# Kernel optimization log

Hardware: AMD Instinct MI355X
Metric: run time of the kernel (lower is better)

## Reference

```python
import jax, jax.numpy as jnp
import numpy as np

N_USER = 100000
N_ITEM = 50000
EMB = 64
LAYERS = 3
N_INTER = 2000000
BATCH = 4096


def setup_inputs() -> dict:
    key = jax.random.key(0)
    ks = jax.random.split(key, 12)
    N = N_USER + N_ITEM
    # bipartite interactions u -> i, symmetrized
    u = jax.random.randint(ks[0], (N_INTER,), 0, N_USER, dtype=jnp.int32)
    i = jax.random.randint(ks[1], (N_INTER,), 0, N_ITEM, dtype=jnp.int32) + N_USER
    edge_src = jnp.concatenate([u, i])
    edge_dst = jnp.concatenate([i, u])
    # symmetric normalization D^-1/2 A D^-1/2 (as in getSparseGraph)
    deg = jnp.bincount(edge_dst, length=N).astype(jnp.float32)
    d_inv_sqrt = jnp.where(deg > 0, jax.lax.rsqrt(jnp.maximum(deg, 1.0)), 0.0)
    edge_w = d_inv_sqrt[edge_src] * d_inv_sqrt[edge_dst]
    s = 1.0 / np.sqrt(EMB)  # xavier-ish scale
    inp = {
        "user_emb": jax.random.normal(ks[2], (N_USER, EMB), jnp.float32) * s,
        "item_emb": jax.random.normal(ks[3], (N_ITEM, EMB), jnp.float32) * s,
        "W_gc": jax.random.normal(ks[4], (LAYERS, EMB, EMB), jnp.float32) * s,
        "b_gc": jax.random.normal(ks[5], (LAYERS, 1, EMB), jnp.float32) * s,
        "W_bi": jax.random.normal(ks[6], (LAYERS, EMB, EMB), jnp.float32) * s,
        "b_bi": jax.random.normal(ks[7], (LAYERS, 1, EMB), jnp.float32) * s,
        "edge_w": edge_w,
        "edge_src": edge_src,
        "edge_dst": edge_dst,
        "users": jax.random.randint(ks[8], (BATCH,), 0, N_USER, dtype=jnp.int64),
        "pos_items": jax.random.randint(ks[9], (BATCH,), 0, N_ITEM, dtype=jnp.int64),
        "neg_items": jax.random.randint(ks[10], (BATCH,), 0, N_ITEM, dtype=jnp.int64),
    }
    return inp


def reference(user_emb, item_emb, W_gc, b_gc, W_bi, b_bi, edge_w,
              edge_src, edge_dst, users, pos_items, neg_items):
    n_user = user_emb.shape[0]
    N = n_user + item_emb.shape[0]
    ego = jnp.concatenate([user_emb, item_emb], axis=0)  # [N, d]
    all_embeddings = [ego]
    for k in range(W_gc.shape[0]):
        # SpMM: side = A_hat @ ego  (gather + weighted scatter-add)
        side = jax.ops.segment_sum(ego[edge_src] * edge_w[:, None], edge_dst,
                                   num_segments=N)
        sum_e = side @ W_gc[k] + b_gc[k]
        bi_e = (ego * side) @ W_bi[k] + b_bi[k]
        ego = jax.nn.leaky_relu(sum_e + bi_e, negative_slope=0.2)
        # dropout omitted (eval mode / identity for deterministic baseline)
        nrm = jnp.linalg.norm(ego, axis=1, keepdims=True)
        all_embeddings.append(ego / jnp.maximum(nrm, 1e-12))
    all_e = jnp.concatenate(all_embeddings, axis=1)  # [N, (L+1)*d]
    u_g = all_e[:n_user][users]
    i_g = all_e[n_user:]
    return (u_g, i_g[pos_items], i_g[neg_items])
```

## Files before the change

kernel.cpp:

```cpp
#include <hip/hip_runtime.h>

#define EMB 64
#define B2SHIFT 8
#define B2ROWS 256
#define MAXB 1024

typedef short v8s __attribute__((ext_vector_type(8)));
typedef float v4f __attribute__((ext_vector_type(4)));

__device__ __forceinline__ float b2f(unsigned short u) {
    return __uint_as_float(((unsigned int)u) << 16);
}
__device__ __forceinline__ float b2f_lo(unsigned int u) {
    return __uint_as_float(u << 16);
}
__device__ __forceinline__ float b2f_hi(unsigned int u) {
    return __uint_as_float(u & 0xFFFF0000u);
}
__device__ __forceinline__ unsigned short f2b(float f) {
    unsigned int u = __float_as_uint(f);
    u += 0x7FFF + ((u >> 16) & 1);
    return (unsigned short)(u >> 16);
}

__global__ void k_init_ego(const float* __restrict__ user_emb,
                           const float* __restrict__ item_emb,
                           const float* __restrict__ dsq,
                           unsigned short* __restrict__ egob,
                           unsigned short* __restrict__ egow,
                           unsigned short* __restrict__ all_eb,
                           int n_user, int N) {
    int idx = blockIdx.x * blockDim.x + threadIdx.x;
    int total = N * 16;
    if (idx >= total) return;
    int n = idx >> 4;
    int q = idx & 15;
    float4 v = (n < n_user)
        ? ((const float4*)user_emb)[idx]
        : ((const float4*)item_emb)[(size_t)(n - n_user) * 16 + q];
    float dn = dsq[n];
    unsigned int pb0 = (unsigned)f2b(v.x) | ((unsigned)f2b(v.y) << 16);
    unsigned int pb1 = (unsigned)f2b(v.z) | ((unsigned)f2b(v.w) << 16);
    unsigned int pw0 = (unsigned)f2b(dn * v.x) | ((unsigned)f2b(dn * v.y) << 16);
    unsigned int pw1 = (unsigned)f2b(dn * v.z) | ((unsigned)f2b(dn * v.w) << 16);
    unsigned int* egobd = (unsigned int*)egob;
    unsigned int* egowd = (unsigned int*)egow;
    egobd[idx * 2 + 0] = pb0;
    egobd[idx * 2 + 1] = pb1;
    egowd[idx * 2 + 0] = pw0;
    egowd[idx * 2 + 1] = pw1;
    unsigned int* ae = (unsigned int*)all_eb;
    __builtin_nontemporal_store(pb0, &ae[(size_t)n * 128 + q * 2 + 0]);
    __builtin_nontemporal_store(pb1, &ae[(size_t)n * 128 + q * 2 + 1]);
}

__global__ __launch_bounds__(256) void k_bhist(const int* __restrict__ dst,
                                               int* __restrict__ bins,
                                               int M, int nb2) {
    __shared__ int h[MAXB];
    for (int i = threadIdx.x; i < nb2; i += 256) h[i] = 0;
    __syncthreads();
    for (int e = blockIdx.x * 256 + threadIdx.x; e < M; e += gridDim.x * 256)
        atomicAdd(&h[dst[e] >> B2SHIFT], 1);
    __syncthreads();
    for (int i = threadIdx.x; i < nb2; i += 256)
        if (h[i]) atomicAdd(&bins[i], h[i]);
}

__global__ __launch_bounds__(1024) void k_bscan(const int* __restrict__ bins,
                                                int* __restrict__ boff,
                                                int* __restrict__ bcur,
                                                int* __restrict__ row_ptr,
                                                int P, int N) {
    __shared__ int buf[1024];
    int tid = threadIdx.x;
    int v = (tid < P) ? bins[tid] : 0;
    buf[tid] = v;
    __syncthreads();
    for (int d = 1; d < 1024; d <<= 1) {
        int add = (tid >= d) ? buf[tid - d] : 0;
        __syncthreads();
        buf[tid] += add;
        __syncthreads();
    }
    if (tid < P) {
        int excl = buf[tid] - v;
        boff[tid] = excl;
        bcur[tid] = excl;
    }
    if (tid == P - 1) {
        boff[P] = buf[tid];
        row_ptr[N] = buf[tid];
    }
}

__global__ __launch_bounds__(256) void k_bin(const int* __restrict__ src,
                                             const int* __restrict__ dst,
                                             int* __restrict__ bcur,
                                             int* __restrict__ binned,
                                             int M, int nb2) {
    __shared__ int hist[MAXB];
    __shared__ int runcur[MAXB];
    int chunk = (M + gridDim.x - 1) / gridDim.x;
    int lo = blockIdx.x * chunk;
    int hi = min(lo + chunk, M);
    for (int i = threadIdx.x; i < nb2; i += 256) hist[i] = 0;
    __syncthreads();
    for (int e = lo + threadIdx.x; e < hi; e += 256)
        atomicAdd(&hist[dst[e] >> B2SHIFT], 1);
    __syncthreads();
    for (int i = threadIdx.x; i < nb2; i += 256) {
        int c = hist[i];
        runcur[i] = c ? atomicAdd(&bcur[i], c) : 0;
    }
    __syncthreads();
    for (int e = lo + threadIdx.x; e < hi; e += 256) {
        int d = dst[e];
        int pos = atomicAdd(&runcur[d >> B2SHIFT], 1);
        binned[pos] = (src[e] << B2SHIFT) | (d & (B2ROWS - 1));
    }
}

__global__ __launch_bounds__(256) void k_csrb(const int* __restrict__ boff,
                                              const int* __restrict__ binned,
                                              int* __restrict__ row_ptr,
                                              float* __restrict__ dsq,
                                              int* __restrict__ csr, int N) {
    __shared__ int hist[B2ROWS];
    __shared__ int scan[B2ROWS];
    int b = blockIdx.x;
    int beg = boff[b], end = boff[b + 1];
    int tid = threadIdx.x;
    hist[tid] = 0;
    __syncthreads();
    for (int e = beg + tid; e < end; e += 256)
        atomicAdd(&hist[binned[e] & (B2ROWS - 1)], 1);
    __syncthreads();
    int c = hist[tid];
    scan[tid] = c;
    __syncthreads();
    for (int d = 1; d < B2ROWS; d <<= 1) {
        int add = (tid >= d) ? scan[tid - d] : 0;
        __syncthreads();
        scan[tid] += add;
        __syncthreads();
    }
    int excl = beg + scan[tid] - c;
    int node = (b << B2SHIFT) + tid;
    if (node < N) {
        row_ptr[node] = excl;
        dsq[node] = (c > 0) ? rsqrtf((float)c) : 0.0f;
    }
    __syncthreads();
    hist[tid] = excl;
    __syncthreads();
    for (int e = beg + tid; e < end; e += 256) {
        int v = binned[e];
        int pos = atomicAdd(&hist[v & (B2ROWS - 1)], 1);
        csr[pos] = v >> B2SHIFT;
    }
}

__global__ __launch_bounds__(256) void k_side(const int* __restrict__ row_ptr,
                                              const int* __restrict__ csr,
                                              const float* __restrict__ dsq,
                                              const unsigned short* __restrict__ egow,
                                              const unsigned short* __restrict__ egob,
                                              unsigned short* __restrict__ X, int N) {
    int wave = threadIdx.x >> 6;
    int lane = threadIdx.x & 63;
    int n = blockIdx.x * 4 + wave;
    if (n >= N) return;
    int beg = __builtin_amdgcn_readfirstlane(row_ptr[n]);
    int end = __builtin_amdgcn_readfirstlane(row_ptr[n + 1]);
    float a0 = 0.f, a1 = 0.f, a2 = 0.f, a3 = 0.f;
    int e = beg;
    for (; e + 16 <= end; e += 16) {
        int s0  = csr[e + 0],  s1  = csr[e + 1],  s2  = csr[e + 2],  s3  = csr[e + 3];
        int s4  = csr[e + 4],  s5  = csr[e + 5],  s6  = csr[e + 6],  s7  = csr[e + 7];
        int s8  = csr[e + 8],  s9  = csr[e + 9],  s10 = csr[e + 10], s11 = csr[e + 11];
        int s12 = csr[e + 12], s13 = csr[e + 13], s14 = csr[e + 14], s15 = csr[e + 15];
        float v0  = b2f(egow[(size_t)s0  * EMB + lane]);
        float v1  = b2f(egow[(size_t)s1  * EMB + lane]);
        float v2  = b2f(egow[(size_t)s2  * EMB + lane]);
        float v3  = b2f(egow[(size_t)s3  * EMB + lane]);
        float v4  = b2f(egow[(size_t)s4  * EMB + lane]);
        float v5  = b2f(egow[(size_t)s5  * EMB + lane]);
        float v6  = b2f(egow[(size_t)s6  * EMB + lane]);
        float v7  = b2f(egow[(size_t)s7  * EMB + lane]);
        float v8  = b2f(egow[(size_t)s8  * EMB + lane]);
        float v9  = b2f(egow[(size_t)s9  * EMB + lane]);
        float v10 = b2f(egow[(size_t)s10 * EMB + lane]);
        float v11 = b2f(egow[(size_t)s11 * EMB + lane]);
        float v12 = b2f(egow[(size_t)s12 * EMB + lane]);
        float v13 = b2f(egow[(size_t)s13 * EMB + lane]);
        float v14 = b2f(egow[(size_t)s14 * EMB + lane]);
        float v15 = b2f(egow[(size_t)s15 * EMB + lane]);
        a0 += v0;  a1 += v1;  a2 += v2;  a3 += v3;
        a0 += v4;  a1 += v5;  a2 += v6;  a3 += v7;
        a0 += v8;  a1 += v9;  a2 += v10; a3 += v11;
        a0 += v12; a1 += v13; a2 += v14; a3 += v15;
    }
    for (; e + 4 <= end; e += 4) {
        int s0 = csr[e + 0], s1 = csr[e + 1], s2 = csr[e + 2], s3 = csr[e + 3];
        float v0 = b2f(egow[(size_t)s0 * EMB + lane]);
        float v1 = b2f(egow[(size_t)s1 * EMB + lane]);
        float v2 = b2f(egow[(size_t)s2 * EMB + lane]);
        float v3 = b2f(egow[(size_t)s3 * EMB + lane]);
        a0 += v0; a1 += v1; a2 += v2; a3 += v3;
    }
    for (; e < end; ++e) {
        int s0 = csr[e];
        a0 += b2f(egow[(size_t)s0 * EMB + lane]);
    }
    float s = dsq[n] * ((a0 + a1) + (a2 + a3));
    float eg = b2f(egob[(size_t)n * EMB + lane]);
    X[(size_t)n * 128 + lane] = f2b(s);
    X[(size_t)n * 128 + 64 + lane] = f2b(s * eg);
}

__global__ __launch_bounds__(256, 2) void k_mt(
        const unsigned short* __restrict__ X,
        unsigned short* __restrict__ egob, unsigned short* __restrict__ egow,
        const float* __restrict__ dsq,
        const float* __restrict__ Wgc, const float* __restrict__ bgc,
        const float* __restrict__ Wbi, const float* __restrict__ bbi,
        unsigned short* __restrict__ all_eb, int N, int layer_col,
        int write_next) {
    __shared__ unsigned short sWT[64 * 136];
    __shared__ __align__(16) float sB[64];
    int tid = threadIdx.x;
    for (int i = tid; i < 64 * 64; i += 256) {
        int k = i >> 6, n = i & 63;
        sWT[n * 136 + k]      = f2b(Wgc[i]);
        sWT[n * 136 + 64 + k] = f2b(Wbi[i]);
    }
    if (tid < 64) sB[tid] = bgc[tid] + bbi[tid];
    __syncthreads();

    int wave = tid >> 6, lane = tid & 63;
    int q = lane >> 4, col = lane & 15;

    v8s Bf[4][4];
#pragma unroll
    for (int nt = 0; nt < 4; nt++)
#pragma unroll
        for (int kt = 0; kt < 4; kt++)
            Bf[nt][kt] = *(const v8s*)&sWT[(nt * 16 + col) * 136 + kt * 32 + q * 8];
    float4 bias[4];
#pragma unroll
    for (int nt = 0; nt < 4; nt++)
        bias[nt] = ((const float4*)sB)[nt * 4 + q];

    int nrt = (N + 15) >> 4;
    int rt0 = (blockIdx.x * 4 + wave) * 4;
    int rt1 = min(rt0 + 4, nrt);
    for (int t = rt0; t < rt1; t++) {
        int r0 = t << 4;
        int rowA = min(r0 + col, N - 1);
        v8s Af[4];
#pragma unroll
        for (int kt = 0; kt < 4; kt++)
            Af[kt] = *(const v8s*)&X[(size_t)rowA * 128 + kt * 32 + q * 8];
        v4f acc[4];
#pragma unroll
        for (int nt = 0; nt < 4; nt++)
            acc[nt] = (v4f){bias[nt].x, bias[nt].y, bias[nt].z, bias[nt].w};
#pragma unroll
        for (int kt = 0; kt < 4; kt++)
#pragma unroll
            for (int nt = 0; nt < 4; nt++)
                acc[nt] = __builtin_amdgcn_mfma_f32_16x16x32_bf16(
                    Bf[nt][kt], Af[kt], acc[nt], 0, 0, 0);
        int row = r0 + col;
        float vv[4][4];
        float ssq = 0.f;
#pragma unroll
        for (int nt = 0; nt < 4; nt++)
#pragma unroll
            for (int rg = 0; rg < 4; rg++) {
                float x = acc[nt][rg];
                x = x > 0.f ? x : 0.2f * x;
                vv[nt][rg] = x;
                ssq += x * x;
            }
        ssq += __shfl_xor(ssq, 16, 64);
        ssq += __shfl_xor(ssq, 32, 64);
        float inv = 1.0f / fmaxf(sqrtf(ssq), 1e-12f);
        if (row < N) {
            unsigned int* ae = (unsigned int*)all_eb;
            size_t aeBase = (size_t)row * 128 + (layer_col >> 1);
#pragma unroll
            for (int nt = 0; nt < 4; nt++) {
                int cd = (nt * 16 + q * 4) >> 1;
                unsigned int p0 = (unsigned)f2b(vv[nt][0] * inv) |
                                  ((unsigned)f2b(vv[nt][1] * inv) << 16);
                unsigned int p1 = (unsigned)f2b(vv[nt][2] * inv) |
                                  ((unsigned)f2b(vv[nt][3] * inv) << 16);
                __builtin_nontemporal_store(p0, &ae[aeBase + cd + 0]);
                __builtin_nontemporal_store(p1, &ae[aeBase + cd + 1]);
            }
            if (write_next) {
                float dn = dsq[row];
                unsigned int* eb = (unsigned int*)egob;
                unsigned int* ew = (unsigned int*)egow;
                size_t base = (size_t)row * 32;
#pragma unroll
                for (int nt = 0; nt < 4; nt++) {
                    int cd = (nt * 16 + q * 4) >> 1;
                    unsigned int b0 = (unsigned)f2b(vv[nt][0]) |
                                      ((unsigned)f2b(vv[nt][1]) << 16);
                    unsigned int b1 = (unsigned)f2b(vv[nt][2]) |
                                      ((unsigned)f2b(vv[nt][3]) << 16);
                    eb[base + cd + 0] = b0;
                    eb[base + cd + 1] = b1;
                    unsigned int w0 = (unsigned)f2b(vv[nt][0] * dn) |
                                      ((unsigned)f2b(vv[nt][1] * dn) << 16);
                    unsigned int w1 = (unsigned)f2b(vv[nt][2] * dn) |
                                      ((unsigned)f2b(vv[nt][3] * dn) << 16);
                    ew[base + cd + 0] = w0;
                    ew[base + cd + 1] = w1;
                }
            }
        }
    }
}

__global__ void k_gather(const unsigned short* __restrict__ all_eb,
                         const int* __restrict__ users,
                         const int* __restrict__ pos,
                         const int* __restrict__ neg,
                         float* __restrict__ out, int n_user, int batch) {
    int idx = blockIdx.x * blockDim.x + threadIdx.x;
    int total = batch * 64;
    if (idx >= 3 * total) return;
    int which = idx / total;
    int r = idx - which * total;
    int b = r >> 6;
    int q = r & 63;
    int node;
    if (which == 0) node = users[b];
    else if (which == 1) node = n_user + pos[b];
    else node = n_user + neg[b];
    const unsigned int* ae = (const unsigned int*)all_eb;
    unsigned int d0 = ae[(size_t)node * 128 + q * 2 + 0];
    unsigned int d1 = ae[(size_t)node * 128 + q * 2 + 1];
    float4 o;
    o.x = b2f_lo(d0);
    o.y = b2f_hi(d0);
    o.z = b2f_lo(d1);
    o.w = b2f_hi(d1);
    ((float4*)out)[idx] = o;
}

static inline size_t align256(size_t x) { return (x + 255) & ~(size_t)255; }

extern "C" void kernel_launch(void* const* d_in, const int* in_sizes, int n_in,
                              void* d_out, int out_size, void* d_ws, size_t ws_size,
                              hipStream_t stream) {
    const float* user_emb = (const float*)d_in[0];
    const float* item_emb = (const float*)d_in[1];
    const float* W_gc = (const float*)d_in[2];
    const float* b_gc = (const float*)d_in[3];
    const float* W_bi = (const float*)d_in[4];
    const float* b_bi = (const float*)d_in[5];
    const int* edge_src = (const int*)d_in[7];
    const int* edge_dst = (const int*)d_in[8];
    const int* users = (const int*)d_in[9];
    const int* pos = (const int*)d_in[10];
    const int* neg = (const int*)d_in[11];

    int n_user = in_sizes[0] / EMB;
    int n_item = in_sizes[1] / EMB;
    int N = n_user + n_item;
    int M = in_sizes[6];
    int layers = in_sizes[2] / (EMB * EMB);
    int batch = in_sizes[9];
    float* out = (float*)d_out;

    int nb2 = (N + B2ROWS - 1) >> B2SHIFT;
    int nrt = (N + 15) >> 4;

    char* p = (char*)d_ws;
    unsigned short* egob = (unsigned short*)p;   p += align256((size_t)N * EMB * 2);
    unsigned short* egow = (unsigned short*)p;   p += align256((size_t)N * EMB * 2);
    unsigned short* X = (unsigned short*)p;      p += align256((size_t)N * 128 * 2);
    unsigned short* all_eb = (unsigned short*)p; p += align256((size_t)N * 256 * 2);
    float* dsq = (float*)p;            p += align256((size_t)N * 4);
    int* row_ptr = (int*)p;            p += align256((size_t)(N + 1) * 4);
    int* bins = (int*)p;               p += align256((size_t)nb2 * 4);
    int* boff = (int*)p;               p += align256((size_t)(nb2 + 1) * 4);
    int* bcur = (int*)p;               p += align256((size_t)nb2 * 4);
    int* binned = (int*)p;             p += align256((size_t)M * 4);
    int* csr = (int*)p;                p += align256((size_t)M * 4);

    hipMemsetAsync(bins, 0, (size_t)nb2 * 4, stream);

    k_bhist<<<512, 256, 0, stream>>>(edge_dst, bins, M, nb2);
    k_bscan<<<1, 1024, 0, stream>>>(bins, boff, bcur, row_ptr, nb2, N);
    k_bin<<<512, 256, 0, stream>>>(edge_src, edge_dst, bcur, binned, M, nb2);
    k_csrb<<<nb2, 256, 0, stream>>>(boff, binned, row_ptr, dsq, csr, N);

    k_init_ego<<<(N * 16 + 255) / 256, 256, 0, stream>>>(
        user_emb, item_emb, dsq, egob, egow, all_eb, n_user, N);

    for (int k = 0; k < layers; k++) {
        k_side<<<(N + 3) / 4, 256, 0, stream>>>(row_ptr, csr, dsq, egow, egob, X, N);
        k_mt<<<(nrt + 15) / 16, 256, 0, stream>>>(
            X, egob, egow, dsq,
            W_gc + (size_t)k * EMB * EMB, b_gc + (size_t)k * EMB,
            W_bi + (size_t)k * EMB * EMB, b_bi + (size_t)k * EMB,
            all_eb, N, (k + 1) * EMB, (k < layers - 1) ? 1 : 0);
    }

    k_gather<<<(3 * batch * 64 + 255) / 256, 256, 0, stream>>>(
        all_eb, users, pos, neg, out, n_user, batch);
}
```

Baseline: 570.6 us.

## Fuse SpMM gather and MFMA transform into one kernel with ping-pong ego buffers

Merges the per-node neighbor gather kernel and the dense MFMA transform kernel into a single kernel. Each block gathers 16 nodes into LDS and immediately runs the 64x128 by 128x64 bf16 MFMA, with the four waves splitting the output columns and reducing the row norms through LDS. This removes the intermediate X buffer round trip through global memory and one launch per layer, and double-buffers the ego arrays so reads and writes don't alias. In exchange, every block re-converts the full weight matrix into LDS, and each wave now handles only one 16-column slice.

```diff
diff --git a/kernel.cpp b/kernel.cpp
--- a/kernel.cpp
+++ b/kernel.cpp
@@ -161,18 +161,9 @@
     }
 }
 
-__global__ __launch_bounds__(256) void k_side(const int* __restrict__ row_ptr,
-                                              const int* __restrict__ csr,
-                                              const float* __restrict__ dsq,
-                                              const unsigned short* __restrict__ egow,
-                                              const unsigned short* __restrict__ egob,
-                                              unsigned short* __restrict__ X, int N) {
-    int wave = threadIdx.x >> 6;
-    int lane = threadIdx.x & 63;
-    int n = blockIdx.x * 4 + wave;
-    if (n >= N) return;
-    int beg = __builtin_amdgcn_readfirstlane(row_ptr[n]);
-    int end = __builtin_amdgcn_readfirstlane(row_ptr[n + 1]);
+__device__ __forceinline__ float gather_node(const int* __restrict__ csr,
+                                             const unsigned short* __restrict__ egow,
+                                             int beg, int end, int lane) {
     float a0 = 0.f, a1 = 0.f, a2 = 0.f, a3 = 0.f;
     int e = beg;
     for (; e + 16 <= end; e += 16) {
@@ -213,115 +204,104 @@
         int s0 = csr[e];
         a0 += b2f(egow[(size_t)s0 * EMB + lane]);
     }
-    float s = dsq[n] * ((a0 + a1) + (a2 + a3));
-    float eg = b2f(egob[(size_t)n * EMB + lane]);
-    X[(size_t)n * 128 + lane] = f2b(s);
-    X[(size_t)n * 128 + 64 + lane] = f2b(s * eg);
-}
-
-__global__ __launch_bounds__(256, 2) void k_mt(
-        const unsigned short* __restrict__ X,
-        unsigned short* __restrict__ egob, unsigned short* __restrict__ egow,
+    return (a0 + a1) + (a2 + a3);
+}
+
+__global__ __launch_bounds__(256, 2) void k_fused(
+        const int* __restrict__ row_ptr, const int* __restrict__ csr,
         const float* __restrict__ dsq,
+        const unsigned short* __restrict__ egob_in,
+        const unsigned short* __restrict__ egow_in,
+        unsigned short* __restrict__ egob_out,
+        unsigned short* __restrict__ egow_out,
         const float* __restrict__ Wgc, const float* __restrict__ bgc,
         const float* __restrict__ Wbi, const float* __restrict__ bbi,
         unsigned short* __restrict__ all_eb, int N, int layer_col,
         int write_next) {
     __shared__ unsigned short sWT[64 * 136];
+    __shared__ __align__(16) unsigned short sX[16 * 136];
     __shared__ __align__(16) float sB[64];
+    __shared__ float sS[4][16];
     int tid = threadIdx.x;
+    int wave = tid >> 6, lane = tid & 63;
+
     for (int i = tid; i < 64 * 64; i += 256) {
         int k = i >> 6, n = i & 63;
         sWT[n * 136 + k]      = f2b(Wgc[i]);
         sWT[n * 136 + 64 + k] = f2b(Wbi[i]);
     }
     if (tid < 64) sB[tid] = bgc[tid] + bbi[tid];
-    __syncthreads();
-
-    int wave = tid >> 6, lane = tid & 63;
+
+    int base_n = (blockIdx.x << 4) + wave * 4;
+#pragma unroll
+    for (int j = 0; j < 4; ++j) {
+        int n = base_n + j;
+        int r = wave * 4 + j;
+        if (n < N) {
+            int beg = __builtin_amdgcn_readfirstlane(row_ptr[n]);
+            int end = __builtin_amdgcn_readfirstlane(row_ptr[n + 1]);
+            float sum = gather_node(csr, egow_in, beg, end, lane);
+            float s = dsq[n] * sum;
+            float eg = b2f(egob_in[(size_t)n * EMB + lane]);
+            sX[r * 136 + lane] = f2b(s);
+            sX[r * 136 + 64 + lane] = f2b(s * eg);
+        } else {
+            sX[r * 136 + lane] = 0;
+            sX[r * 136 + 64 + lane] = 0;
+        }
+    }
+    __syncthreads();
+
     int q = lane >> 4, col = lane & 15;
-
-    v8s Bf[4][4];
-#pragma unroll
-    for (int nt = 0; nt < 4; nt++)
-#pragma unroll
-        for (int kt = 0; kt < 4; kt++)
-            Bf[nt][kt] = *(const v8s*)&sWT[(nt * 16 + col) * 136 + kt * 32 + q * 8];
-    float4 bias[4];
-#pragma unroll
-    for (int nt = 0; nt < 4; nt++)
-        bias[nt] = ((const float4*)sB)[nt * 4 + q];
-
-    int nrt = (N + 15) >> 4;
-    int rt0 = (blockIdx.x * 4 + wave) * 4;
-    int rt1 = min(rt0 + 4, nrt);
-    for (int t = rt0; t < rt1; t++) {
-        int r0 = t << 4;
-        int rowA = min(r0 + col, N - 1);
-        v8s Af[4];
-#pragma unroll
-        for (int kt = 0; kt < 4; kt++)
-            Af[kt] = *(const v8s*)&X[(size_t)rowA * 128 + kt * 32 + q * 8];
-        v4f acc[4];
-#pragma unroll
-        for (int nt = 0; nt < 4; nt++)
-            acc[nt] = (v4f){bias[nt].x, bias[nt].y, bias[nt].z, bias[nt].w};
-#pragma unroll
-        for (int kt = 0; kt < 4; kt++)
-#pragma unroll
-            for (int nt = 0; nt < 4; nt++)
-                acc[nt] = __builtin_amdgcn_mfma_f32_16x16x32_bf16(
-                    Bf[nt][kt], Af[kt], acc[nt], 0, 0, 0);
-        int row = r0 + col;
-        float vv[4][4];
-        float ssq = 0.f;
-#pragma unroll
-        for (int nt = 0; nt < 4; nt++)
-#pragma unroll
-            for (int rg = 0; rg < 4; rg++) {
-                float x = acc[nt][rg];
-                x = x > 0.f ? x : 0.2f * x;
-                vv[nt][rg] = x;
-                ssq += x * x;
-            }
-        ssq += __shfl_xor(ssq, 16, 64);
-        ssq += __shfl_xor(ssq, 32, 64);
-        float inv = 1.0f / fmaxf(sqrtf(ssq), 1e-12f);
-        if (row < N) {
-            unsigned int* ae = (unsigned int*)all_eb;
-            size_t aeBase = (size_t)row * 128 + (layer_col >> 1);
-#pragma unroll
-            for (int nt = 0; nt < 4; nt++) {
-                int cd = (nt * 16 + q * 4) >> 1;
-                unsigned int p0 = (unsigned)f2b(vv[nt][0] * inv) |
-                                  ((unsigned)f2b(vv[nt][1] * inv) << 16);
-                unsigned int p1 = (unsigned)f2b(vv[nt][2] * inv) |
-                                  ((unsigned)f2b(vv[nt][3] * inv) << 16);
-                __builtin_nontemporal_store(p0, &ae[aeBase + cd + 0]);
-                __builtin_nontemporal_store(p1, &ae[aeBase + cd + 1]);
-            }
-            if (write_next) {
-                float dn = dsq[row];
-                unsigned int* eb = (unsigned int*)egob;
-                unsigned int* ew = (unsigned int*)egow;
-                size_t base = (size_t)row * 32;
-#pragma unroll
-                for (int nt = 0; nt < 4; nt++) {
-                    int cd = (nt * 16 + q * 4) >> 1;
-                    unsigned int b0 = (unsigned)f2b(vv[nt][0]) |
-                                      ((unsigned)f2b(vv[nt][1]) << 16);
-                    unsigned int b1 = (unsigned)f2b(vv[nt][2]) |
-                                      ((unsigned)f2b(vv[nt][3]) << 16);
-                    eb[base + cd + 0] = b0;
-                    eb[base + cd + 1] = b1;
-                    unsigned int w0 = (unsigned)f2b(vv[nt][0] * dn) |
-                                      ((unsigned)f2b(vv[nt][1] * dn) << 16);
-                    unsigned int w1 = (unsigned)f2b(vv[nt][2] * dn) |
-                                      ((unsigned)f2b(vv[nt][3] * dn) << 16);
-                    ew[base + cd + 0] = w0;
-                    ew[base + cd + 1] = w1;
-                }
-            }
+    v8s Bf0 = *(const v8s*)&sWT[(wave * 16 + col) * 136 + 0 * 32 + q * 8];
+    v8s Bf1 = *(const v8s*)&sWT[(wave * 16 + col) * 136 + 1 * 32 + q * 8];
+    v8s Bf2 = *(const v8s*)&sWT[(wave * 16 + col) * 136 + 2 * 32 + q * 8];
+    v8s Bf3 = *(const v8s*)&sWT[(wave * 16 + col) * 136 + 3 * 32 + q * 8];
+    v8s Af0 = *(const v8s*)&sX[col * 136 + 0 * 32 + q * 8];
+    v8s Af1 = *(const v8s*)&sX[col * 136 + 1 * 32 + q * 8];
+    v8s Af2 = *(const v8s*)&sX[col * 136 + 2 * 32 + q * 8];
+    v8s Af3 = *(const v8s*)&sX[col * 136 + 3 * 32 + q * 8];
+    float4 bias4 = ((const float4*)sB)[wave * 4 + q];
+    v4f acc = (v4f){bias4.x, bias4.y, bias4.z, bias4.w};
+    acc = __builtin_amdgcn_mfma_f32_16x16x32_bf16(Bf0, Af0, acc, 0, 0, 0);
+    acc = __builtin_amdgcn_mfma_f32_16x16x32_bf16(Bf1, Af1, acc, 0, 0, 0);
+    acc = __builtin_amdgcn_mfma_f32_16x16x32_bf16(Bf2, Af2, acc, 0, 0, 0);
+    acc = __builtin_amdgcn_mfma_f32_16x16x32_bf16(Bf3, Af3, acc, 0, 0, 0);
+
+    float vv0 = acc[0] > 0.f ? acc[0] : 0.2f * acc[0];
+    float vv1 = acc[1] > 0.f ? acc[1] : 0.2f * acc[1];
+    float vv2 = acc[2] > 0.f ? acc[2] : 0.2f * acc[2];
+    float vv3 = acc[3] > 0.f ? acc[3] : 0.2f * acc[3];
+    float ssq = vv0 * vv0 + vv1 * vv1 + vv2 * vv2 + vv3 * vv3;
+    ssq += __shfl_xor(ssq, 16, 64);
+    ssq += __shfl_xor(ssq, 32, 64);
+    if (lane < 16) sS[wave][lane] = ssq;
+    __syncthreads();
+    float tot = sS[0][col] + sS[1][col] + sS[2][col] + sS[3][col];
+    float inv = 1.0f / fmaxf(sqrtf(tot), 1e-12f);
+
+    int row = (blockIdx.x << 4) + col;
+    if (row < N) {
+        unsigned int* ae = (unsigned int*)all_eb;
+        size_t aeBase = (size_t)row * 128 + (layer_col >> 1);
+        int cd = (wave * 16 + q * 4) >> 1;
+        unsigned int p0 = (unsigned)f2b(vv0 * inv) | ((unsigned)f2b(vv1 * inv) << 16);
+        unsigned int p1 = (unsigned)f2b(vv2 * inv) | ((unsigned)f2b(vv3 * inv) << 16);
+        __builtin_nontemporal_store(p0, &ae[aeBase + cd + 0]);
+        __builtin_nontemporal_store(p1, &ae[aeBase + cd + 1]);
+        if (write_next) {
+            float dn = dsq[row];
+            unsigned int* eb = (unsigned int*)egob_out;
+            unsigned int* ew = (unsigned int*)egow_out;
+            size_t base = (size_t)row * 32;
+            unsigned int b0 = (unsigned)f2b(vv0) | ((unsigned)f2b(vv1) << 16);
+            unsigned int b1 = (unsigned)f2b(vv2) | ((unsigned)f2b(vv3) << 16);
+            eb[base + cd + 0] = b0;
+            eb[base + cd + 1] = b1;
+            unsigned int w0 = (unsigned)f2b(vv0 * dn) | ((unsigned)f2b(vv1 * dn) << 16);
+            unsigned int w1 = (unsigned)f2b(vv2 * dn) | ((unsigned)f2b(vv3 * dn) << 16);
+            ew[base + cd + 0] = w0;
+            ew[base + cd + 1] = w1;
         }
     }
 }
@@ -382,9 +362,10 @@
     int nrt = (N + 15) >> 4;
 
     char* p = (char*)d_ws;
-    unsigned short* egob = (unsigned short*)p;   p += align256((size_t)N * EMB * 2);
-    unsigned short* egow = (unsigned short*)p;   p += align256((size_t)N * EMB * 2);
-    unsigned short* X = (unsigned short*)p;      p += align256((size_t)N * 128 * 2);
+    unsigned short* egob0 = (unsigned short*)p;  p += align256((size_t)N * EMB * 2);
+    unsigned short* egow0 = (unsigned short*)p;  p += align256((size_t)N * EMB * 2);
+    unsigned short* egob1 = (unsigned short*)p;  p += align256((size_t)N * EMB * 2);
+    unsigned short* egow1 = (unsigned short*)p;  p += align256((size_t)N * EMB * 2);
     unsigned short* all_eb = (unsigned short*)p; p += align256((size_t)N * 256 * 2);
     float* dsq = (float*)p;            p += align256((size_t)N * 4);
     int* row_ptr = (int*)p;            p += align256((size_t)(N + 1) * 4);
@@ -402,12 +383,15 @@
     k_csrb<<<nb2, 256, 0, stream>>>(boff, binned, row_ptr, dsq, csr, N);
 
     k_init_ego<<<(N * 16 + 255) / 256, 256, 0, stream>>>(
-        user_emb, item_emb, dsq, egob, egow, all_eb, n_user, N);
+        user_emb, item_emb, dsq, egob0, egow0, all_eb, n_user, N);
 
     for (int k = 0; k < layers; k++) {
-        k_side<<<(N + 3) / 4, 256, 0, stream>>>(row_ptr, csr, dsq, egow, egob, X, N);
-        k_mt<<<(nrt + 15) / 16, 256, 0, stream>>>(
-            X, egob, egow, dsq,
+        const unsigned short* ebi = (k & 1) ? egob1 : egob0;
+        const unsigned short* ewi = (k & 1) ? egow1 : egow0;
+        unsigned short* ebo = (k & 1) ? egob0 : egob1;
+        unsigned short* ewo = (k & 1) ? egow0 : egow1;
+        k_fused<<<nrt, 256, 0, stream>>>(
+            row_ptr, csr, dsq, ebi, ewi, ebo, ewo,
             W_gc + (size_t)k * EMB * EMB, b_gc + (size_t)k * EMB,
             W_bi + (size_t)k * EMB * EMB, b_bi + (size_t)k * EMB,
             all_eb, N, (k + 1) * EMB, (k < layers - 1) ? 1 : 0);
```

Measured after the change: 574.5 us. Within noise of the previous version (+0.7%).
